# Kernel tuning notes

Hardware: AMD Instinct MI355X
Metric: run time of the kernel (lower is better)

The kernel has to match this reference:

```python
import jax, jax.numpy as jnp
import numpy as np

N = 100000
E = 1600000
IN_C = 128
HID = 128
EMB = 64
EPS = 1e-5


def setup_inputs() -> dict:
    key = jax.random.key(0)
    ks = jax.random.split(key, 8)
    x = jax.random.normal(ks[0], (N, IN_C), dtype=jnp.float32)
    edge_index = jax.random.randint(ks[1], (2, E), 0, N, dtype=jnp.int64)
    s1 = 1.0 / np.sqrt(IN_C)
    s2 = 1.0 / np.sqrt(HID)
    # SAGEConv layer 1: lin_l (aggregated neighbors, with bias), lin_r (root, no bias)
    W1l = jax.random.uniform(ks[2], (IN_C, HID), jnp.float32, -s1, s1)
    b1 = jnp.zeros((HID,), jnp.float32)
    W1r = jax.random.uniform(ks[3], (IN_C, HID), jnp.float32, -s1, s1)
    g1 = jnp.ones((HID,), jnp.float32)
    be1 = jnp.zeros((HID,), jnp.float32)
    # SAGEConv layer 2
    W2l = jax.random.uniform(ks[4], (HID, EMB), jnp.float32, -s2, s2)
    b2 = jnp.zeros((EMB,), jnp.float32)
    W2r = jax.random.uniform(ks[5], (HID, EMB), jnp.float32, -s2, s2)
    g2 = jnp.ones((EMB,), jnp.float32)
    be2 = jnp.zeros((EMB,), jnp.float32)
    return {"x": x, "edge_index": edge_index,
            "W1l": W1l, "b1": b1, "W1r": W1r, "g1": g1, "be1": be1,
            "W2l": W2l, "b2": b2, "W2r": W2r, "g2": g2, "be2": be2}


def _mean_aggregate(x, src, dst, n_nodes):
    # mean of source-node features over incoming edges at each dst node
    msg_sum = jax.ops.segment_sum(x[src], dst, num_segments=n_nodes)  # [N, C]
    cnt = jax.ops.segment_sum(jnp.ones((src.shape[0],), x.dtype), dst,
                              num_segments=n_nodes)
    return msg_sum / jnp.maximum(cnt, 1.0)[:, None]


def _sage_conv(x, src, dst, Wl, b, Wr):
    agg = _mean_aggregate(x, src, dst, x.shape[0])
    return agg @ Wl + b + x @ Wr


def _batch_norm_eval(x, gamma, beta):
    # eval-mode BN with running_mean=0, running_var=1
    return x * (gamma / jnp.sqrt(1.0 + EPS)) + beta


def reference(x, edge_index, W1l, b1, W1r, g1, be1, W2l, b2, W2r, g2, be2):
    src, dst = edge_index[0], edge_index[1]
    h = _sage_conv(x, src, dst, W1l, b1, W1r)
    h = jax.nn.relu(_batch_norm_eval(h, g1, be1))  # dropout is identity in eval
    h = _sage_conv(h, src, dst, W2l, b2, W2r)
    h = jax.nn.relu(_batch_norm_eval(h, g2, be2))
    return h
```

## Files before the change

kernel.cpp:

```cpp
#include <hip/hip_runtime.h>
#include <math.h>

#define EPS 1e-5f
#define BSH 9
#define BSPAN 512
#define CHUNK 2048
#define CAP 16384

typedef __attribute__((ext_vector_type(8))) short short8;
typedef __attribute__((ext_vector_type(4))) float f32x4;
typedef __attribute__((ext_vector_type(2))) float f32x2;

__device__ __forceinline__ short f2bf(float f) {
  union { float f; unsigned u; } v; v.f = f;
  unsigned r = v.u + 0x7fff + ((v.u >> 16) & 1);
  return (short)(r >> 16);
}

__global__ __launch_bounds__(256) void k_prep(
    const float* __restrict__ x, unsigned short* __restrict__ xbf,
    unsigned* __restrict__ xf8, long long n8,
    const int* __restrict__ ei, int* __restrict__ bcnt, int E, int n,
    int ncast, int nhist,
    const float* __restrict__ W1l, const float* __restrict__ W1r,
    short* __restrict__ wp1,
    const float* __restrict__ W2l, const float* __restrict__ W2r,
    short* __restrict__ wp2) {
  __shared__ int h[256];
  int b = blockIdx.x, tid = threadIdx.x;
  if (b < ncast) {
    long long i = (long long)b * 256 + tid;
    if (i < n8) {
      const float4* p = (const float4*)x + i * 2;
      float4 v0 = p[0], v1 = p[1];
      short8 o;
      o[0] = f2bf(v0.x); o[1] = f2bf(v0.y); o[2] = f2bf(v0.z); o[3] = f2bf(v0.w);
      o[4] = f2bf(v1.x); o[5] = f2bf(v1.y); o[6] = f2bf(v1.z); o[7] = f2bf(v1.w);
      ((short8*)xbf)[i] = o;
      unsigned lo = __builtin_amdgcn_cvt_pk_fp8_f32(v0.x, v0.y, 0u, false);
      lo = __builtin_amdgcn_cvt_pk_fp8_f32(v0.z, v0.w, lo, true);
      unsigned hi = __builtin_amdgcn_cvt_pk_fp8_f32(v1.x, v1.y, 0u, false);
      hi = __builtin_amdgcn_cvt_pk_fp8_f32(v1.z, v1.w, hi, true);
      ((uint2*)xf8)[i] = make_uint2(lo, hi);
    }
  } else if (b < ncast + nhist) {
    h[tid] = 0;
    __syncthreads();
    long long base = (long long)(b - ncast) * CHUNK;
#pragma unroll
    for (int i = 0; i < CHUNK / 256; ++i) {
      long long e = base + i * 256 + tid;
      if (e < E) {
        int d = ei[E + e];
        if ((unsigned)d < (unsigned)n) atomicAdd(&h[d >> BSH], 1);
      }
    }
    __syncthreads();
    if (h[tid]) atomicAdd(&bcnt[tid], h[tid]);
  } else if (b < ncast + nhist + 16) {
    int t = (b - ncast - nhist) * 256 + tid;
    int l = t & 63, f = t >> 6;
    int kt = f >> 3, ct = f & 7;
    int c = ct * 16 + (l & 15);
    int kb = kt * 32 + (l >> 4) * 8;
    short8 v;
#pragma unroll
    for (int j = 0; j < 8; ++j) {
      int k = kb + j;
      float w = (k < 128) ? W1l[k * 128 + c] : W1r[(k - 128) * 128 + c];
      v[j] = f2bf(w);
    }
    *(short8*)(wp1 + (size_t)t * 8) = v;
  } else {
    int t = (b - ncast - nhist - 16) * 256 + tid;
    int l = t & 63, f = t >> 6;
    int kt = f >> 3, ct = f & 7;
    int c = ct * 16 + (l & 15);
    int kb = kt * 32 + (l >> 4) * 8;
    short8 v;
#pragma unroll
    for (int j = 0; j < 8; ++j) {
      int k = kb + j;
      float w = (c < 64) ? W2l[k * 64 + c] : W2r[k * 64 + (c - 64)];
      v[j] = f2bf(w);
    }
    *(short8*)(wp2 + (size_t)t * 8) = v;
  }
}

__global__ __launch_bounds__(256) void k_bscan(
    const int* __restrict__ bcnt, int* __restrict__ bbase,
    int* __restrict__ bcur, int nbk) {
  __shared__ int s[256];
  int t = threadIdx.x;
  int v = (t < nbk) ? bcnt[t] : 0;
  s[t] = v;
  __syncthreads();
  for (int off = 1; off < 256; off <<= 1) {
    int xv = (t >= off) ? s[t - off] : 0;
    __syncthreads();
    s[t] += xv;
    __syncthreads();
  }
  int excl = s[t] - v;
  if (t < nbk) { bbase[t] = excl; bcur[t] = excl; }
}

__global__ __launch_bounds__(256) void k_scatter(
    const int* __restrict__ ei, int* __restrict__ bcur,
    unsigned* __restrict__ epk, int E, int n) {
  __shared__ int h[256];
  __shared__ int base[256];
  int tid = threadIdx.x;
  h[tid] = 0;
  __syncthreads();
  long long cbase = (long long)blockIdx.x * CHUNK;
  int src[CHUNK / 256], dl[CHUNK / 256], rk[CHUNK / 256], bk[CHUNK / 256];
#pragma unroll
  for (int i = 0; i < CHUNK / 256; ++i) {
    long long e = cbase + i * 256 + tid;
    bk[i] = -1;
    if (e < E) {
      int s = ei[e], d = ei[E + e];
      if ((unsigned)d < (unsigned)n) {
        bk[i] = d >> BSH; dl[i] = d & (BSPAN - 1); src[i] = s;
        rk[i] = atomicAdd(&h[bk[i]], 1);
      }
    }
  }
  __syncthreads();
  base[tid] = h[tid] ? atomicAdd(&bcur[tid], h[tid]) : 0;
  __syncthreads();
#pragma unroll
  for (int i = 0; i < CHUNK / 256; ++i) {
    if (bk[i] >= 0)
      epk[base[bk[i]] + rk[i]] = ((unsigned)dl[i] << 18) | (unsigned)src[i];
  }
}

__global__ __launch_bounds__(256) void k_build(
    const unsigned* __restrict__ epk, const int* __restrict__ bbase,
    const int* __restrict__ bcnt, int* __restrict__ rowptr,
    int* __restrict__ ssrc, int n, int nbk) {
  __shared__ int cnt[BSPAN];
  __shared__ int rp[BSPAN];
  __shared__ int cur[BSPAN];
  __shared__ int lsrc[CAP];
  int b = blockIdx.x, t = threadIdx.x;
  int segbase = bbase[b], segcnt = bcnt[b];
  int i0 = t, i1 = t + 256;
  cnt[i0] = 0; cnt[i1] = 0;
  __syncthreads();
  for (int i = t; i < segcnt; i += 256)
    atomicAdd(&cnt[epk[segbase + i] >> 18], 1);
  __syncthreads();
  rp[i0] = cnt[i0]; rp[i1] = cnt[i1];
  __syncthreads();
  for (int off = 1; off < BSPAN; off <<= 1) {
    int v0 = (i0 >= off) ? rp[i0 - off] : 0;
    int v1 = (i1 >= off) ? rp[i1 - off] : 0;
    __syncthreads();
    rp[i0] += v0; rp[i1] += v1;
    __syncthreads();
  }
  int e0 = rp[i0] - cnt[i0], e1 = rp[i1] - cnt[i1];
  cur[i0] = e0; cur[i1] = e1;
  int node0 = b * BSPAN;
  if (node0 + i0 < n) rowptr[node0 + i0] = segbase + e0;
  if (node0 + i1 < n) rowptr[node0 + i1] = segbase + e1;
  if (b == nbk - 1 && t == 0) rowptr[n] = segbase + segcnt;
  __syncthreads();
  if (segcnt <= CAP) {
    for (int i = t; i < segcnt; i += 256) {
      unsigned k = epk[segbase + i];
      int pos = atomicAdd(&cur[k >> 18], 1);
      lsrc[pos] = (int)(k & 0x3FFFFu);
    }
    __syncthreads();
    for (int i = t; i < segcnt; i += 256) ssrc[segbase + i] = lsrc[i];
  } else {
    for (int i = t; i < segcnt; i += 256) {
      unsigned k = epk[segbase + i];
      int pos = atomicAdd(&cur[k >> 18], 1);
      ssrc[segbase + pos] = (int)(k & 0x3FFFFu);
    }
  }
}

__global__ __launch_bounds__(256) void k_agg1(
    const int* __restrict__ rowptr, const int* __restrict__ ssrc,
    const unsigned* __restrict__ xf8, unsigned short* __restrict__ aggbf,
    int n) {
  int w = (blockIdx.x * 256 + threadIdx.x) >> 6;
  if (w >= n) return;
  int l = threadIdx.x & 63;
  int q = l >> 4, ql = l & 15;
  int beg = rowptr[w], end = rowptr[w + 1];
  f32x2 a01 = {0.f, 0.f}, a23 = {0.f, 0.f}, a45 = {0.f, 0.f}, a67 = {0.f, 0.f};
  const uint2* xb2 = (const uint2*)xf8;
  int endm1 = end - 1;
  for (int p = beg + q; p < end; p += 16) {
    int i1 = p + 4, i2 = p + 8, i3 = p + 12;
    int j1 = min(i1, endm1), j2 = min(i2, endm1), j3 = min(i3, endm1);
    int s0 = ssrc[p], s1 = ssrc[j1], s2 = ssrc[j2], s3 = ssrc[j3];
    uint2 v0 = xb2[(size_t)s0 * 16 + ql];
    uint2 v1 = xb2[(size_t)s1 * 16 + ql];
    uint2 v2 = xb2[(size_t)s2 * 16 + ql];
    uint2 v3 = xb2[(size_t)s3 * 16 + ql];
    if (i1 > endm1) { v1.x = 0u; v1.y = 0u; }
    if (i2 > endm1) { v2.x = 0u; v2.y = 0u; }
    if (i3 > endm1) { v3.x = 0u; v3.y = 0u; }
    a01 += __builtin_amdgcn_cvt_pk_f32_fp8(v0.x, false);
    a23 += __builtin_amdgcn_cvt_pk_f32_fp8(v0.x, true);
    a45 += __builtin_amdgcn_cvt_pk_f32_fp8(v0.y, false);
    a67 += __builtin_amdgcn_cvt_pk_f32_fp8(v0.y, true);
    a01 += __builtin_amdgcn_cvt_pk_f32_fp8(v1.x, false);
    a23 += __builtin_amdgcn_cvt_pk_f32_fp8(v1.x, true);
    a45 += __builtin_amdgcn_cvt_pk_f32_fp8(v1.y, false);
    a67 += __builtin_amdgcn_cvt_pk_f32_fp8(v1.y, true);
    a01 += __builtin_amdgcn_cvt_pk_f32_fp8(v2.x, false);
    a23 += __builtin_amdgcn_cvt_pk_f32_fp8(v2.x, true);
    a45 += __builtin_amdgcn_cvt_pk_f32_fp8(v2.y, false);
    a67 += __builtin_amdgcn_cvt_pk_f32_fp8(v2.y, true);
    a01 += __builtin_amdgcn_cvt_pk_f32_fp8(v3.x, false);
    a23 += __builtin_amdgcn_cvt_pk_f32_fp8(v3.x, true);
    a45 += __builtin_amdgcn_cvt_pk_f32_fp8(v3.y, false);
    a67 += __builtin_amdgcn_cvt_pk_f32_fp8(v3.y, true);
  }
  float a[8] = {a01[0], a01[1], a23[0], a23[1], a45[0], a45[1], a67[0], a67[1]};
#pragma unroll
  for (int j = 0; j < 8; ++j) {
    a[j] += __shfl_xor(a[j], 16, 64);
    a[j] += __shfl_xor(a[j], 32, 64);
  }
  if (q == 0) {
    float inv = 1.0f / fmaxf((float)(end - beg), 1.0f);
    uint4 o;
    o.x = ((unsigned)(unsigned short)f2bf(a[1] * inv) << 16)
        | (unsigned short)f2bf(a[0] * inv);
    o.y = ((unsigned)(unsigned short)f2bf(a[3] * inv) << 16)
        | (unsigned short)f2bf(a[2] * inv);
    o.z = ((unsigned)(unsigned short)f2bf(a[5] * inv) << 16)
        | (unsigned short)f2bf(a[4] * inv);
    o.w = ((unsigned)(unsigned short)f2bf(a[7] * inv) << 16)
        | (unsigned short)f2bf(a[6] * inv);
    ((uint4*)aggbf)[(size_t)w * 16 + ql] = o;
  }
}

__global__ __launch_bounds__(256) void k_lin1(
    const unsigned short* __restrict__ xbf,
    const unsigned short* __restrict__ aggbf,
    const short* __restrict__ wp, const float* __restrict__ b,
    const float* __restrict__ g, const float* __restrict__ be,
    unsigned short* __restrict__ h1bf, int n) {
  __shared__ short As[64 * 256];
  int tid = threadIdx.x;
  int row0 = blockIdx.x * 64;
#pragma unroll
  for (int it = 0; it < 8; ++it) {
    int slot = it * 256 + tid;
    int r = slot >> 5;
    int c16 = slot & 31;
    int gr = row0 + r;
    short8 o = {0, 0, 0, 0, 0, 0, 0, 0};
    if (gr < n) {
      const unsigned short* src = (c16 < 16)
          ? (aggbf + (size_t)gr * 128 + c16 * 8)
          : (xbf + (size_t)gr * 128 + (c16 - 16) * 8);
      o = *(const short8*)src;
    }
    int byte = r * 512 + ((c16 * 16) ^ ((r & 7) << 4));
    *(short8*)((char*)As + byte) = o;
  }
  __syncthreads();
  int w = tid >> 6, l = tid & 63;
  int rloc = w * 16 + (l & 15);
  f32x4 acc[8];
#pragma unroll
  for (int i = 0; i < 8; ++i) acc[i] = (f32x4){0.f, 0.f, 0.f, 0.f};
#pragma unroll
  for (int kt = 0; kt < 8; ++kt) {
    int abyte = rloc * 512 + ((kt * 64 + (l >> 4) * 16) ^ ((rloc & 7) << 4));
    short8 a = *(short8*)((char*)As + abyte);
#pragma unroll
    for (int ct = 0; ct < 8; ++ct) {
      short8 bf = *(const short8*)(wp + ((size_t)((kt * 8 + ct) * 64 + l)) * 8);
      acc[ct] = __builtin_amdgcn_mfma_f32_16x16x32_bf16(a, bf, acc[ct], 0, 0, 0);
    }
  }
  int rbase = row0 + w * 16 + (l >> 4) * 4;
  int cb = l & 15;
#pragma unroll
  for (int ct = 0; ct < 8; ++ct) {
    int c = ct * 16 + cb;
    float sc = g[c] * (1.0f / sqrtf(1.0f + EPS));
    float bb = b[c], bt = be[c];
#pragma unroll
    for (int q = 0; q < 4; ++q) {
      int r = rbase + q;
      if (r < n) {
        float v = (acc[ct][q] + bb) * sc + bt;
        h1bf[(size_t)r * 128 + c] = (unsigned short)f2bf(fmaxf(v, 0.f));
      }
    }
  }
}

__global__ __launch_bounds__(256) void k_lin2(
    const unsigned short* __restrict__ h1bf, const short* __restrict__ wp,
    const float* __restrict__ b2,
    unsigned char* __restrict__ yf8, float* __restrict__ pre, int n) {
  __shared__ short As[64 * 128];
  int tid = threadIdx.x;
  int row0 = blockIdx.x * 64;
#pragma unroll
  for (int it = 0; it < 4; ++it) {
    int slot = it * 256 + tid;
    int r = slot >> 4;
    int c16 = slot & 15;
    int gr = row0 + r;
    short8 o = {0, 0, 0, 0, 0, 0, 0, 0};
    if (gr < n) o = *(const short8*)(h1bf + (size_t)gr * 128 + c16 * 8);
    int byte = r * 256 + ((c16 * 16) ^ ((r & 7) << 4));
    *(short8*)((char*)As + byte) = o;
  }
  __syncthreads();
  int w = tid >> 6, l = tid & 63;
  int rloc = w * 16 + (l & 15);
  f32x4 acc[8];
#pragma unroll
  for (int i = 0; i < 8; ++i) acc[i] = (f32x4){0.f, 0.f, 0.f, 0.f};
#pragma unroll
  for (int kt = 0; kt < 4; ++kt) {
    int abyte = rloc * 256 + ((kt * 64 + (l >> 4) * 16) ^ ((rloc & 7) << 4));
    short8 a = *(short8*)((char*)As + abyte);
#pragma unroll
    for (int ct = 0; ct < 8; ++ct) {
      short8 bf = *(const short8*)(wp + ((size_t)((kt * 8 + ct) * 64 + l)) * 8);
      acc[ct] = __builtin_amdgcn_mfma_f32_16x16x32_bf16(a, bf, acc[ct], 0, 0, 0);
    }
  }
  int rbase = row0 + w * 16 + (l >> 4) * 4;
  int cb = l & 15;
#pragma unroll
  for (int ct = 0; ct < 8; ++ct) {
    int c = ct * 16 + cb;
#pragma unroll
    for (int q = 0; q < 4; ++q) {
      int r = rbase + q;
      if (r < n) {
        if (c < 64) {
          unsigned pk = __builtin_amdgcn_cvt_pk_fp8_f32(
              acc[ct][q], acc[ct][q], 0u, false);
          yf8[(size_t)r * 64 + c] = (unsigned char)pk;
        } else {
          pre[(size_t)r * 64 + (c - 64)] = acc[ct][q] + b2[c - 64];
        }
      }
    }
  }
}

__global__ __launch_bounds__(256) void k_agg2(
    const int* __restrict__ rowptr, const int* __restrict__ ssrc,
    const unsigned* __restrict__ yf8, const float* __restrict__ g,
    const float* __restrict__ be, float* __restrict__ out, int n) {
  int w = (blockIdx.x * 256 + threadIdx.x) >> 6;
  if (w >= n) return;
  int l = threadIdx.x & 63;
  int q = l >> 4, ql = l & 15;
  int beg = rowptr[w], end = rowptr[w + 1];
  f32x2 a01 = {0.f, 0.f}, a23 = {0.f, 0.f};
  int endm1 = end - 1;
  for (int p = beg + q; p < end; p += 16) {
    int i1 = p + 4, i2 = p + 8, i3 = p + 12;
    int j1 = min(i1, endm1), j2 = min(i2, endm1), j3 = min(i3, endm1);
    int s0 = ssrc[p], s1 = ssrc[j1], s2 = ssrc[j2], s3 = ssrc[j3];
    unsigned v0 = yf8[(size_t)s0 * 16 + ql];
    unsigned v1 = yf8[(size_t)s1 * 16 + ql];
    unsigned v2 = yf8[(size_t)s2 * 16 + ql];
    unsigned v3 = yf8[(size_t)s3 * 16 + ql];
    if (i1 > endm1) v1 = 0u;
    if (i2 > endm1) v2 = 0u;
    if (i3 > endm1) v3 = 0u;
    a01 += __builtin_amdgcn_cvt_pk_f32_fp8(v0, false);
    a23 += __builtin_amdgcn_cvt_pk_f32_fp8(v0, true);
    a01 += __builtin_amdgcn_cvt_pk_f32_fp8(v1, false);
    a23 += __builtin_amdgcn_cvt_pk_f32_fp8(v1, true);
    a01 += __builtin_amdgcn_cvt_pk_f32_fp8(v2, false);
    a23 += __builtin_amdgcn_cvt_pk_f32_fp8(v2, true);
    a01 += __builtin_amdgcn_cvt_pk_f32_fp8(v3, false);
    a23 += __builtin_amdgcn_cvt_pk_f32_fp8(v3, true);
  }
  float a0 = a01[0], a1 = a01[1], a2 = a23[0], a3 = a23[1];
  a0 += __shfl_xor(a0, 16, 64); a0 += __shfl_xor(a0, 32, 64);
  a1 += __shfl_xor(a1, 16, 64); a1 += __shfl_xor(a1, 32, 64);
  a2 += __shfl_xor(a2, 16, 64); a2 += __shfl_xor(a2, 32, 64);
  a3 += __shfl_xor(a3, 16, 64); a3 += __shfl_xor(a3, 32, 64);
  if (q == 0) {
    float inv = 1.0f / fmaxf((float)(end - beg), 1.0f);
    float rr = 1.0f / sqrtf(1.0f + EPS);
    float4 gv = ((const float4*)g)[ql];
    float4 bv = ((const float4*)be)[ql];
    float4 po = ((const float4*)out)[(size_t)w * 16 + ql];
    float4 v;
    v.x = fmaxf((a0 * inv + po.x) * (gv.x * rr) + bv.x, 0.f);
    v.y = fmaxf((a1 * inv + po.y) * (gv.y * rr) + bv.y, 0.f);
    v.z = fmaxf((a2 * inv + po.z) * (gv.z * rr) + bv.z, 0.f);
    v.w = fmaxf((a3 * inv + po.w) * (gv.w * rr) + bv.w, 0.f);
    ((float4*)out)[(size_t)w * 16 + ql] = v;
  }
}

extern "C" void kernel_launch(void* const* d_in, const int* in_sizes, int n_in,
                              void* d_out, int out_size, void* d_ws, size_t ws_size,
                              hipStream_t stream) {
  const float* x   = (const float*)d_in[0];
  const int*   ei  = (const int*)d_in[1];
  const float* W1l = (const float*)d_in[2];
  const float* b1  = (const float*)d_in[3];
  const float* W1r = (const float*)d_in[4];
  const float* g1  = (const float*)d_in[5];
  const float* be1 = (const float*)d_in[6];
  const float* W2l = (const float*)d_in[7];
  const float* b2  = (const float*)d_in[8];
  const float* W2r = (const float*)d_in[9];
  const float* g2  = (const float*)d_in[10];
  const float* be2 = (const float*)d_in[11];
  float* out = (float*)d_out;

  int n = in_sizes[0] / 128;
  int E = in_sizes[1] / 2;
  int nbk = (n + BSPAN - 1) / BSPAN;
  int nce = (int)(((long long)E + CHUNK - 1) / CHUNK);
  long long n8 = (long long)n * 16;
  int ncast = (int)((n8 + 255) / 256);

  char* ws = (char*)d_ws;
  size_t o = 0;
  auto carve = [&](size_t bytes) {
    char* p = ws + o;
    o += (bytes + 255) & ~(size_t)255;
    return p;
  };
  int*      bcnt   = (int*)carve(256 * 4);
  int*      bbase  = (int*)carve(256 * 4);
  int*      bcur   = (int*)carve(256 * 4);
  unsigned* epk    = (unsigned*)carve((size_t)E * 4);
  int*      ssrc   = (int*)carve((size_t)E * 4);
  int*      rowptr = (int*)carve((size_t)(n + 1) * 4);
  short*    wp1    = (short*)carve((size_t)64 * 64 * 8 * 2);
  short*    wp2    = (short*)carve((size_t)32 * 64 * 8 * 2);
  unsigned short* xbf   = (unsigned short*)carve((size_t)n * 128 * 2);
  unsigned*       xf8   = (unsigned*)carve((size_t)n * 128);
  unsigned short* aggbf = (unsigned short*)carve((size_t)n * 128 * 2);
  unsigned short* h1bf  = (unsigned short*)carve((size_t)n * 128 * 2);
  unsigned char*  yf8   = (unsigned char*)carve((size_t)n * 64);

  hipMemsetAsync(bcnt, 0, 256 * 4, stream);

  k_prep<<<ncast + nce + 24, 256, 0, stream>>>(
      x, xbf, xf8, n8, ei, bcnt, E, n, ncast, nce,
      W1l, W1r, wp1, W2l, W2r, wp2);
  k_bscan<<<1, 256, 0, stream>>>(bcnt, bbase, bcur, nbk);
  k_scatter<<<nce, 256, 0, stream>>>(ei, bcur, epk, E, n);
  k_build<<<nbk, 256, 0, stream>>>(epk, bbase, bcnt, rowptr, ssrc, n, nbk);

  {
    long long T = (long long)n * 64;
    k_agg1<<<(int)((T + 255) / 256), 256, 0, stream>>>(
        rowptr, ssrc, xf8, aggbf, n);
  }
  k_lin1<<<(n + 63) / 64, 256, 0, stream>>>(xbf, aggbf, wp1, b1, g1, be1, h1bf, n);
  k_lin2<<<(n + 63) / 64, 256, 0, stream>>>(h1bf, wp2, b2, yf8, out, n);
  {
    long long T = (long long)n * 64;
    k_agg2<<<(int)((T + 255) / 256), 256, 0, stream>>>(
        rowptr, ssrc, (const unsigned*)yf8, g2, be2, out, n);
  }
}
```

Baseline: 213.5 us.

## Pad CSR neighbor lists to multiples of 16 with zero-row sentinel

Builds a padded CSR where each node's neighbor list is rounded up to a multiple of 16 and filled with a sentinel index pointing to an extra zeroed feature row. The aggregation kernels then drop their bounds clamps and masking, and use 32-bit index math. k_build now runs 512 threads per block with one node per thread. The cost is extra gather traffic on padded slots (average degree 16 adds roughly half a row of padding per node), more sentinel writes, and two extra memsets.

Measured after the change: 216.9 us. Within noise of the previous version (+1.6%).

```diff
diff --git a/kernel.cpp b/kernel.cpp
--- a/kernel.cpp
+++ b/kernel.cpp
@@ -6,6 +6,7 @@
 #define BSPAN 512
 #define CHUNK 2048
 #define CAP 16384
+#define MAXPAD (BSPAN * 15)
 
 typedef __attribute__((ext_vector_type(8))) short short8;
 typedef __attribute__((ext_vector_type(4))) float f32x4;
@@ -90,7 +91,7 @@
 
 __global__ __launch_bounds__(256) void k_bscan(
     const int* __restrict__ bcnt, int* __restrict__ bbase,
-    int* __restrict__ bcur, int nbk) {
+    int* __restrict__ bcur, int* __restrict__ pbbase, int nbk) {
   __shared__ int s[256];
   int t = threadIdx.x;
   int v = (t < nbk) ? bcnt[t] : 0;
@@ -103,7 +104,10 @@
     __syncthreads();
   }
   int excl = s[t] - v;
-  if (t < nbk) { bbase[t] = excl; bcur[t] = excl; }
+  if (t < nbk) {
+    bbase[t] = excl; bcur[t] = excl;
+    pbbase[t] = excl + t * MAXPAD;
+  }
 }
 
 __global__ __launch_bounds__(256) void k_scatter(
@@ -138,78 +142,80 @@
   }
 }
 
-__global__ __launch_bounds__(256) void k_build(
+__global__ __launch_bounds__(512) void k_build(
     const unsigned* __restrict__ epk, const int* __restrict__ bbase,
-    const int* __restrict__ bcnt, int* __restrict__ rowptr,
-    int* __restrict__ ssrc, int n, int nbk) {
-  __shared__ int cnt[BSPAN];
+    const int* __restrict__ pbbase, const int* __restrict__ bcnt,
+    int* __restrict__ deg, int* __restrict__ prow,
+    int* __restrict__ pssrc, int n, int nbk) {
   __shared__ int rp[BSPAN];
   __shared__ int cur[BSPAN];
+  __shared__ int cnt[BSPAN];
   __shared__ int lsrc[CAP];
   int b = blockIdx.x, t = threadIdx.x;
   int segbase = bbase[b], segcnt = bcnt[b];
-  int i0 = t, i1 = t + 256;
-  cnt[i0] = 0; cnt[i1] = 0;
-  __syncthreads();
-  for (int i = t; i < segcnt; i += 256)
+  int psegbase = pbbase[b];
+  cnt[t] = 0;
+  __syncthreads();
+  for (int i = t; i < segcnt; i += 512)
     atomicAdd(&cnt[epk[segbase + i] >> 18], 1);
   __syncthreads();
-  rp[i0] = cnt[i0]; rp[i1] = cnt[i1];
+  int d = cnt[t];
+  int pd = (d + 15) & ~15;
+  rp[t] = pd;
   __syncthreads();
   for (int off = 1; off < BSPAN; off <<= 1) {
-    int v0 = (i0 >= off) ? rp[i0 - off] : 0;
-    int v1 = (i1 >= off) ? rp[i1 - off] : 0;
-    __syncthreads();
-    rp[i0] += v0; rp[i1] += v1;
-    __syncthreads();
-  }
-  int e0 = rp[i0] - cnt[i0], e1 = rp[i1] - cnt[i1];
-  cur[i0] = e0; cur[i1] = e1;
-  int node0 = b * BSPAN;
-  if (node0 + i0 < n) rowptr[node0 + i0] = segbase + e0;
-  if (node0 + i1 < n) rowptr[node0 + i1] = segbase + e1;
-  if (b == nbk - 1 && t == 0) rowptr[n] = segbase + segcnt;
-  __syncthreads();
-  if (segcnt <= CAP) {
-    for (int i = t; i < segcnt; i += 256) {
+    int v = (t >= off) ? rp[t - off] : 0;
+    __syncthreads();
+    rp[t] += v;
+    __syncthreads();
+  }
+  int pe0 = rp[t] - pd;
+  cur[t] = pe0;
+  int node = b * BSPAN + t;
+  if (node < n) { deg[node] = d; prow[node] = psegbase + pe0; }
+  int ptotal = rp[BSPAN - 1];
+  __syncthreads();
+  if (ptotal <= CAP) {
+    for (int i = t; i < ptotal; i += 512) lsrc[i] = n;
+    __syncthreads();
+    for (int i = t; i < segcnt; i += 512) {
       unsigned k = epk[segbase + i];
       int pos = atomicAdd(&cur[k >> 18], 1);
       lsrc[pos] = (int)(k & 0x3FFFFu);
     }
     __syncthreads();
-    for (int i = t; i < segcnt; i += 256) ssrc[segbase + i] = lsrc[i];
+    for (int i = t; i < ptotal; i += 512) pssrc[psegbase + i] = lsrc[i];
   } else {
-    for (int i = t; i < segcnt; i += 256) {
+    for (int i = t; i < ptotal; i += 512) pssrc[psegbase + i] = n;
+    __syncthreads();
+    for (int i = t; i < segcnt; i += 512) {
       unsigned k = epk[segbase + i];
       int pos = atomicAdd(&cur[k >> 18], 1);
-      ssrc[segbase + pos] = (int)(k & 0x3FFFFu);
+      pssrc[psegbase + pos] = (int)(k & 0x3FFFFu);
     }
   }
 }
 
 __global__ __launch_bounds__(256) void k_agg1(
-    const int* __restrict__ rowptr, const int* __restrict__ ssrc,
+    const int* __restrict__ prow, const int* __restrict__ deg,
+    const int* __restrict__ pssrc,
     const unsigned* __restrict__ xf8, unsigned short* __restrict__ aggbf,
     int n) {
   int w = (blockIdx.x * 256 + threadIdx.x) >> 6;
   if (w >= n) return;
   int l = threadIdx.x & 63;
   int q = l >> 4, ql = l & 15;
-  int beg = rowptr[w], end = rowptr[w + 1];
+  int d = deg[w];
+  int pbase = prow[w];
+  int pend = pbase + ((d + 15) & ~15);
   f32x2 a01 = {0.f, 0.f}, a23 = {0.f, 0.f}, a45 = {0.f, 0.f}, a67 = {0.f, 0.f};
   const uint2* xb2 = (const uint2*)xf8;
-  int endm1 = end - 1;
-  for (int p = beg + q; p < end; p += 16) {
-    int i1 = p + 4, i2 = p + 8, i3 = p + 12;
-    int j1 = min(i1, endm1), j2 = min(i2, endm1), j3 = min(i3, endm1);
-    int s0 = ssrc[p], s1 = ssrc[j1], s2 = ssrc[j2], s3 = ssrc[j3];
-    uint2 v0 = xb2[(size_t)s0 * 16 + ql];
-    uint2 v1 = xb2[(size_t)s1 * 16 + ql];
-    uint2 v2 = xb2[(size_t)s2 * 16 + ql];
-    uint2 v3 = xb2[(size_t)s3 * 16 + ql];
-    if (i1 > endm1) { v1.x = 0u; v1.y = 0u; }
-    if (i2 > endm1) { v2.x = 0u; v2.y = 0u; }
-    if (i3 > endm1) { v3.x = 0u; v3.y = 0u; }
+  for (int p = pbase + q; p < pend; p += 16) {
+    int s0 = pssrc[p], s1 = pssrc[p + 4], s2 = pssrc[p + 8], s3 = pssrc[p + 12];
+    uint2 v0 = xb2[(unsigned)s0 * 16u + ql];
+    uint2 v1 = xb2[(unsigned)s1 * 16u + ql];
+    uint2 v2 = xb2[(unsigned)s2 * 16u + ql];
+    uint2 v3 = xb2[(unsigned)s3 * 16u + ql];
     a01 += __builtin_amdgcn_cvt_pk_f32_fp8(v0.x, false);
     a23 += __builtin_amdgcn_cvt_pk_f32_fp8(v0.x, true);
     a45 += __builtin_amdgcn_cvt_pk_f32_fp8(v0.y, false);
@@ -234,7 +240,7 @@
     a[j] += __shfl_xor(a[j], 32, 64);
   }
   if (q == 0) {
-    float inv = 1.0f / fmaxf((float)(end - beg), 1.0f);
+    float inv = 1.0f / fmaxf((float)d, 1.0f);
     uint4 o;
     o.x = ((unsigned)(unsigned short)f2bf(a[1] * inv) << 16)
         | (unsigned short)f2bf(a[0] * inv);
@@ -363,27 +369,24 @@
 }
 
 __global__ __launch_bounds__(256) void k_agg2(
-    const int* __restrict__ rowptr, const int* __restrict__ ssrc,
+    const int* __restrict__ prow, const int* __restrict__ deg,
+    const int* __restrict__ pssrc,
     const unsigned* __restrict__ yf8, const float* __restrict__ g,
     const float* __restrict__ be, float* __restrict__ out, int n) {
   int w = (blockIdx.x * 256 + threadIdx.x) >> 6;
   if (w >= n) return;
   int l = threadIdx.x & 63;
   int q = l >> 4, ql = l & 15;
-  int beg = rowptr[w], end = rowptr[w + 1];
+  int d = deg[w];
+  int pbase = prow[w];
+  int pend = pbase + ((d + 15) & ~15);
   f32x2 a01 = {0.f, 0.f}, a23 = {0.f, 0.f};
-  int endm1 = end - 1;
-  for (int p = beg + q; p < end; p += 16) {
-    int i1 = p + 4, i2 = p + 8, i3 = p + 12;
-    int j1 = min(i1, endm1), j2 = min(i2, endm1), j3 = min(i3, endm1);
-    int s0 = ssrc[p], s1 = ssrc[j1], s2 = ssrc[j2], s3 = ssrc[j3];
-    unsigned v0 = yf8[(size_t)s0 * 16 + ql];
-    unsigned v1 = yf8[(size_t)s1 * 16 + ql];
-    unsigned v2 = yf8[(size_t)s2 * 16 + ql];
-    unsigned v3 = yf8[(size_t)s3 * 16 + ql];
-    if (i1 > endm1) v1 = 0u;
-    if (i2 > endm1) v2 = 0u;
-    if (i3 > endm1) v3 = 0u;
+  for (int p = pbase + q; p < pend; p += 16) {
+    int s0 = pssrc[p], s1 = pssrc[p + 4], s2 = pssrc[p + 8], s3 = pssrc[p + 12];
+    unsigned v0 = yf8[(unsigned)s0 * 16u + ql];
+    unsigned v1 = yf8[(unsigned)s1 * 16u + ql];
+    unsigned v2 = yf8[(unsigned)s2 * 16u + ql];
+    unsigned v3 = yf8[(unsigned)s3 * 16u + ql];
     a01 += __builtin_amdgcn_cvt_pk_f32_fp8(v0, false);
     a23 += __builtin_amdgcn_cvt_pk_f32_fp8(v0, true);
     a01 += __builtin_amdgcn_cvt_pk_f32_fp8(v1, false);
@@ -399,7 +402,7 @@
   a2 += __shfl_xor(a2, 16, 64); a2 += __shfl_xor(a2, 32, 64);
   a3 += __shfl_xor(a3, 16, 64); a3 += __shfl_xor(a3, 32, 64);
   if (q == 0) {
-    float inv = 1.0f / fmaxf((float)(end - beg), 1.0f);
+    float inv = 1.0f / fmaxf((float)d, 1.0f);
     float rr = 1.0f / sqrtf(1.0f + EPS);
     float4 gv = ((const float4*)g)[ql];
     float4 bv = ((const float4*)be)[ql];
@@ -447,36 +450,41 @@
   int*      bcnt   = (int*)carve(256 * 4);
   int*      bbase  = (int*)carve(256 * 4);
   int*      bcur   = (int*)carve(256 * 4);
+  int*      pbbase = (int*)carve(256 * 4);
   unsigned* epk    = (unsigned*)carve((size_t)E * 4);
-  int*      ssrc   = (int*)carve((size_t)E * 4);
-  int*      rowptr = (int*)carve((size_t)(n + 1) * 4);
+  int*      pssrc  = (int*)carve(((size_t)E + (size_t)nbk * MAXPAD + 16) * 4);
+  int*      deg    = (int*)carve((size_t)n * 4);
+  int*      prow   = (int*)carve((size_t)n * 4);
   short*    wp1    = (short*)carve((size_t)64 * 64 * 8 * 2);
   short*    wp2    = (short*)carve((size_t)32 * 64 * 8 * 2);
   unsigned short* xbf   = (unsigned short*)carve((size_t)n * 128 * 2);
-  unsigned*       xf8   = (unsigned*)carve((size_t)n * 128);
+  unsigned*       xf8   = (unsigned*)carve((size_t)(n + 1) * 128);
   unsigned short* aggbf = (unsigned short*)carve((size_t)n * 128 * 2);
   unsigned short* h1bf  = (unsigned short*)carve((size_t)n * 128 * 2);
-  unsigned char*  yf8   = (unsigned char*)carve((size_t)n * 64);
+  unsigned char*  yf8   = (unsigned char*)carve((size_t)(n + 1) * 64);
 
   hipMemsetAsync(bcnt, 0, 256 * 4, stream);
+  hipMemsetAsync((char*)xf8 + (size_t)n * 128, 0, 128, stream);
+  hipMemsetAsync(yf8 + (size_t)n * 64, 0, 64, stream);
 
   k_prep<<<ncast + nce + 24, 256, 0, stream>>>(
       x, xbf, xf8, n8, ei, bcnt, E, n, ncast, nce,
       W1l, W1r, wp1, W2l, W2r, wp2);
-  k_bscan<<<1, 256, 0, stream>>>(bcnt, bbase, bcur, nbk);
+  k_bscan<<<1, 256, 0, stream>>>(bcnt, bbase, bcur, pbbase, nbk);
   k_scatter<<<nce, 256, 0, stream>>>(ei, bcur, epk, E, n);
-  k_build<<<nbk, 256, 0, stream>>>(epk, bbase, bcnt, rowptr, ssrc, n, nbk);
+  k_build<<<nbk, 512, 0, stream>>>(epk, bbase, pbbase, bcnt, deg, prow,
+                                   pssrc, n, nbk);
 
   {
     long long T = (long long)n * 64;
     k_agg1<<<(int)((T + 255) / 256), 256, 0, stream>>>(
-        rowptr, ssrc, xf8, aggbf, n);
+        prow, deg, pssrc, xf8, aggbf, n);
   }
   k_lin1<<<(n + 63) / 64, 256, 0, stream>>>(xbf, aggbf, wp1, b1, g1, be1, h1bf, n);
   k_lin2<<<(n + 63) / 64, 256, 0, stream>>>(h1bf, wp2, b2, yf8, out, n);
   {
     long long T = (long long)n * 64;
     k_agg2<<<(int)((T + 255) / 256), 256, 0, stream>>>(
-        rowptr, ssrc, (const unsigned*)yf8, g2, be2, out, n);
-  }
-}
+        prow, deg, pssrc, (const unsigned*)yf8, g2, be2, out, n);
+  }
+}
```
